# Performance work log

Measured on AMD Instinct MI355X. Metric: run time of the kernel, lower is better.

Reference implementation:

```python
import jax, jax.numpy as jnp
import numpy as np

D_MODEL = 1024
D_HEAD = 512
EPS = 1e-6


def setup_inputs() -> dict:
    key = jax.random.key(0)
    ks = jax.random.split(key, 12)
    s = 0.02
    B, T = 8, 2048
    return {
        "x": jax.random.normal(ks[0], (B, T, D_MODEL), dtype=jnp.float32),
        "norm_w": jnp.ones((D_MODEL,), dtype=jnp.float32),
        "Wq": jax.random.normal(ks[1], (D_HEAD, D_MODEL), dtype=jnp.float32) * s,
        "Wk": jax.random.normal(ks[2], (D_HEAD, D_MODEL), dtype=jnp.float32) * s,
        "Wv": jax.random.normal(ks[3], (D_HEAD, D_MODEL), dtype=jnp.float32) * s,
        "wi_w": jax.random.normal(ks[4], (1, D_MODEL), dtype=jnp.float32) * s,
        "wi_b": jnp.zeros((1,), dtype=jnp.float32),
        "wf_w": jax.random.normal(ks[5], (1, D_MODEL), dtype=jnp.float32) * s,
        "wf_b": jnp.zeros((1,), dtype=jnp.float32),
        "Wo": jax.random.normal(ks[6], (D_HEAD, D_MODEL), dtype=jnp.float32) * s,
        "bo": jnp.zeros((D_HEAD,), dtype=jnp.float32),
        "Wout": jax.random.normal(ks[7], (D_MODEL, D_HEAD), dtype=jnp.float32) * s,
    }


def _forward(x, norm_w, Wq, Wk, Wv, wi_w, wi_b, wf_w, wf_b, Wo, bo, Wout):
    B, T, d_model = x.shape
    d = Wq.shape[0]
    scale = 1.0 / jnp.sqrt(jnp.asarray(d, x.dtype))

    # RMSNorm (pre-norm)
    normed = x * jax.lax.rsqrt(jnp.mean(x * x, axis=-1, keepdims=True) + EPS) * norm_w

    # Precompute all per-timestep projections (vectorized over T)
    q = jnp.einsum('btm,dm->btd', normed, Wq) * scale  # (B,T,d)
    k = jnp.einsum('btm,dm->btd', normed, Wk) * scale
    v = jnp.einsum('btm,dm->btd', normed, Wv)
    zi = jnp.einsum('btm,m->bt', normed, wi_w[0]) + wi_b[0]  # (B,T)
    zf = jnp.einsum('btm,m->bt', normed, wf_w[0]) + wf_b[0]
    o = jax.nn.sigmoid(jnp.einsum('btm,dm->btd', normed, Wo) + bo)  # (B,T,d)

    # Time-major for scan
    qT = jnp.moveaxis(q, 1, 0)
    kT = jnp.moveaxis(k, 1, 0)
    vT = jnp.moveaxis(v, 1, 0)
    ziT = jnp.moveaxis(zi, 1, 0)
    zfT = jnp.moveaxis(zf, 1, 0)
    oT = jnp.moveaxis(o, 1, 0)

    C0 = jnp.zeros((B, d, d), x.dtype)
    n0 = jnp.zeros((B, d), x.dtype)
    m0 = jnp.full((B,), -jnp.inf, x.dtype)

    def step(carry, inp):
        C, n, m = carry
        q_t, k_t, v_t, zi_t, zf_t, o_t = inp
        m_t = jnp.maximum(zf_t + m, zi_t)                      # (B,)
        i_p = jnp.exp(zi_t - m_t)
        f_p = jnp.exp(zf_t + m - m_t)
        C_t = f_p[:, None, None] * C + i_p[:, None, None] * (v_t[:, :, None] * k_t[:, None, :])
        n_t = f_p[:, None] * n + i_p[:, None] * k_t
        Cq = jnp.einsum('bij,bj->bi', C_t, q_t)                # (B,d)
        denom = jnp.maximum(jnp.abs(jnp.sum(n_t * q_t, axis=-1, keepdims=True)), 1.0)
        h = o_t * Cq / denom
        return (C_t, n_t, m_t), h

    (C_f, n_f, m_f), hT = jax.lax.scan(step, (C0, n0, m0), (qT, kT, vT, ziT, zfT, oT))
    h = jnp.moveaxis(hT, 0, 1)                                 # (B,T,d)
    out = x + jnp.einsum('btd,md->btm', h, Wout)
    return out


def reference(x, norm_w, Wq, Wk, Wv, wi_w, wi_b, wf_w, wf_b, Wo, bo, Wout):
    return _forward(x, norm_w, Wq, Wk, Wv, wi_w, wi_b, wf_w, wf_b, Wo, bo, Wout)
```

## Files before the change

### kernel.cpp

```cpp
#include <hip/hip_runtime.h>
#include <cstdint>
#include <cmath>

#define T_SEQ 2048
#define NBATCH 8
#define DM 1024
#define DH 512
#define MROWS (NBATCH * T_SEQ)
#define NC 16
#define CL 128

typedef short s8v __attribute__((ext_vector_type(8)));
typedef float f32x4 __attribute__((ext_vector_type(4)));

typedef unsigned int __attribute__((address_space(1))) uint_g;
typedef unsigned int __attribute__((address_space(3))) uint_l;

#define QKSCALE 0.044194173824159216f

__device__ __forceinline__ float b2f(unsigned short s) {
    union { unsigned u; float f; } c; c.u = ((unsigned)s) << 16; return c.f;
}
__device__ __forceinline__ unsigned short f2b(float f) {
    union { float f; unsigned u; } c; c.f = f;
    unsigned r = c.u + 0x7fffu + ((c.u >> 16) & 1u);
    return (unsigned short)(r >> 16);
}
__device__ __forceinline__ void gld_lds16(const void* g, void* l) {
    __builtin_amdgcn_global_load_lds((const uint_g*)g, (uint_l*)l, 16, 0, 0);
}

#define WAITV(N) asm volatile("s_waitcnt vmcnt(" #N ")" ::: "memory")
#define BARSYNC() do { asm volatile("" ::: "memory"); __builtin_amdgcn_s_barrier(); asm volatile("" ::: "memory"); } while (0)

__global__ __launch_bounds__(256) void norm_kernel(
    const float* __restrict__ x, const float* __restrict__ nw,
    const float* __restrict__ wi, const float* __restrict__ wf,
    const float* __restrict__ wib, const float* __restrict__ wfb,
    unsigned short* __restrict__ normed, float* __restrict__ zi, float* __restrict__ zf,
    const float* __restrict__ Wq, const float* __restrict__ Wk,
    const float* __restrict__ Wo, const float* __restrict__ Wv,
    const float* __restrict__ Wout,
    unsigned short* __restrict__ Wcat1, unsigned short* __restrict__ WvB,
    unsigned short* __restrict__ Woutb)
{
    int t = blockIdx.x, tid = threadIdx.x;
    float4 xv = ((const float4*)(x + (size_t)t * DM))[tid];
    float ss = xv.x * xv.x + xv.y * xv.y + xv.z * xv.z + xv.w * xv.w;
#pragma unroll
    for (int m = 1; m < 64; m <<= 1) ss += __shfl_xor(ss, m, 64);
    __shared__ float sred[4];
    __shared__ float sred2[8];
    if ((tid & 63) == 0) sred[tid >> 6] = ss;
    __syncthreads();
    ss = sred[0] + sred[1] + sred[2] + sred[3];
    float rstd = rsqrtf(ss * (1.0f / DM) + 1e-6f);
    float4 nwv = ((const float4*)nw)[tid];
    float n0 = xv.x * rstd * nwv.x, n1 = xv.y * rstd * nwv.y;
    float n2 = xv.z * rstd * nwv.z, n3 = xv.w * rstd * nwv.w;
    ushort4 pk;
    pk.x = f2b(n0); pk.y = f2b(n1); pk.z = f2b(n2); pk.w = f2b(n3);
    ((ushort4*)(normed + (size_t)t * DM))[tid] = pk;
    float4 wiv = ((const float4*)wi)[tid];
    float4 wfv = ((const float4*)wf)[tid];
    float pzi = n0 * wiv.x + n1 * wiv.y + n2 * wiv.z + n3 * wiv.w;
    float pzf = n0 * wfv.x + n1 * wfv.y + n2 * wfv.z + n3 * wfv.w;
#pragma unroll
    for (int m = 1; m < 64; m <<= 1) {
        pzi += __shfl_xor(pzi, m, 64);
        pzf += __shfl_xor(pzf, m, 64);
    }
    if ((tid & 63) == 0) { sred2[tid >> 6] = pzi; sred2[4 + (tid >> 6)] = pzf; }
    __syncthreads();
    if (tid == 0) {
        zi[t] = sred2[0] + sred2[1] + sred2[2] + sred2[3] + wib[0];
        zf[t] = sred2[4] + sred2[5] + sred2[6] + sred2[7] + wfb[0];
    }
    if (tid < 160) {
        int idx = blockIdx.x * 160 + tid;
        if (idx < 1572864) {
            int nrow = idx >> 10;
            float v;
            if      (nrow < 512)  v = Wq[idx];
            else if (nrow < 1024) v = Wk[idx - 512 * 1024];
            else                  v = Wo[idx - 1024 * 1024];
            Wcat1[idx] = f2b(v);
        } else if (idx < 2097152) {
            int j = idx - 1572864;
            WvB[j] = f2b(Wv[j]);
        } else {
            int j = idx - 2097152;
            Woutb[j] = f2b(Wout[j]);
        }
    }
}

__global__ __launch_bounds__(256, 4) void gemm_qkv_ms(
    const unsigned short* __restrict__ normed, const unsigned short* __restrict__ Wcat1,
    const unsigned short* __restrict__ WvB, int K,
    unsigned short* __restrict__ qko, const float* __restrict__ bo,
    unsigned short* __restrict__ vout,
    const float* __restrict__ zi, const float* __restrict__ zf,
    float* __restrict__ u, float* __restrict__ a)
{
    __shared__ unsigned short As[128 * 64];
    __shared__ unsigned short Bs[128 * 64];
    __shared__ float wt[4];
    int tid = threadIdx.x;

    if (blockIdx.x >= 2048) {
        int b = blockIdx.x - 2048, lane = tid & 63, wid = tid >> 6;
        size_t base = (size_t)b * T_SEQ + tid * 8;
        float z_f[8], z_i[8];
        *(float4*)&z_f[0] = *(const float4*)&zf[base];
        *(float4*)&z_f[4] = *(const float4*)&zf[base + 4];
        *(float4*)&z_i[0] = *(const float4*)&zi[base];
        *(float4*)&z_i[4] = *(const float4*)&zi[base + 4];
        float c8[8]; float run = 0.0f;
#pragma unroll
        for (int i = 0; i < 8; ++i) { run += z_f[i]; c8[i] = run; }
        float v = run;
#pragma unroll
        for (int d = 1; d < 64; d <<= 1) {
            float o = __shfl_up(v, d, 64);
            if (lane >= d) v += o;
        }
        if (lane == 63) wt[wid] = v;
        __syncthreads();
        float woff = 0.0f;
        for (int j = 0; j < wid; ++j) woff += wt[j];
        float excl = __shfl_up(v, 1, 64);
        if (lane == 0) excl = 0.0f;
        float pre = woff + excl;
        float uu[8];
#pragma unroll
        for (int i = 0; i < 8; ++i) uu[i] = z_i[i] - (pre + c8[i]);
        *(float4*)&u[base] = *(float4*)&uu[0];
        *(float4*)&u[base + 4] = *(float4*)&uu[4];
        __syncthreads();
        float m8[8]; float rm = -INFINITY;
#pragma unroll
        for (int i = 0; i < 8; ++i) { rm = fmaxf(rm, uu[i]); m8[i] = rm; }
        float mv = rm;
#pragma unroll
        for (int d = 1; d < 64; d <<= 1) {
            float o = __shfl_up(mv, d, 64);
            if (lane >= d) mv = fmaxf(mv, o);
        }
        if (lane == 63) wt[wid] = mv;
        __syncthreads();
        float moff = -INFINITY;
        for (int j = 0; j < wid; ++j) moff = fmaxf(moff, wt[j]);
        float mexcl = __shfl_up(mv, 1, 64);
        if (lane == 0) mexcl = -INFINITY;
        float mpre = fmaxf(moff, mexcl);
        float aa[8];
#pragma unroll
        for (int i = 0; i < 8; ++i) aa[i] = fmaxf(mpre, m8[i]);
        *(float4*)&a[base] = *(float4*)&aa[0];
        *(float4*)&a[base + 4] = *(float4*)&aa[4];
        return;
    }

    int l = tid & 63, w = tid >> 6;
    int wg = (blockIdx.x & 7) * 256 + (blockIdx.x >> 3);
    int job = (wg >= 1536) ? 1 : 0;
    const unsigned short* A;
    const unsigned short* Bw;
    int bm, bn;
    if (job == 0) { A = normed; Bw = Wcat1; bn = wg % 12; bm = wg / 12; }
    else          { int w2 = wg - 1536; A = WvB; Bw = normed; bm = w2 & 3; bn = w2 >> 2; }
    int wr = w >> 1, wc = w & 1;
    f32x4 acc[4][4] = {};
    const size_t abase = (size_t)(bm * 128) * K;
    const size_t bbase = (size_t)(bn * 128) * K;

    for (int ks = 0; ks < K; ks += 64) {
        __syncthreads();
#pragma unroll
        for (int i = 0; i < 4; ++i) {
            int off = (i * 256 + tid) * 8;
            int row = off >> 6, kc = off & 63;
            int kcs = kc ^ ((row & 7) << 3);
            gld_lds16(A + abase + (size_t)row * K + ks + kcs, &As[off]);
            gld_lds16(Bw + bbase + (size_t)row * K + ks + kcs, &Bs[off]);
        }
        __syncthreads();
#pragma unroll
        for (int kk = 0; kk < 2; ++kk) {
            int cbo = kk * 32 + (l >> 4) * 8;
            s8v af[4], bfv[4];
#pragma unroll
            for (int m = 0; m < 4; ++m) {
                int row = wr * 64 + m * 16 + (l & 15);
                af[m] = *(const s8v*)&As[row * 64 + (cbo ^ ((row & 7) << 3))];
            }
#pragma unroll
            for (int n = 0; n < 4; ++n) {
                int row = wc * 64 + n * 16 + (l & 15);
                bfv[n] = *(const s8v*)&Bs[row * 64 + (cbo ^ ((row & 7) << 3))];
            }
#pragma unroll
            for (int m = 0; m < 4; ++m)
#pragma unroll
                for (int n = 0; n < 4; ++n)
                    acc[m][n] = __builtin_amdgcn_mfma_f32_16x16x32_bf16(af[m], bfv[n], acc[m][n], 0, 0, 0);
        }
    }

    if (job == 0) {
#pragma unroll
        for (int m = 0; m < 4; ++m) {
#pragma unroll
            for (int n = 0; n < 4; ++n) {
                int col = bn * 128 + wc * 64 + n * 16 + (l & 15);
#pragma unroll
                for (int r = 0; r < 4; ++r) {
                    int row = bm * 128 + wr * 64 + m * 16 + (l >> 4) * 4 + r;
                    float v = acc[m][n][r];
                    if (col < 1024) v *= QKSCALE;
                    else {
                        float s = v + bo[col - 1024];
                        v = 1.0f / (1.0f + expf(-s));
                    }
                    qko[(size_t)row * 1536 + col] = f2b(v);
                }
            }
        }
    } else {
#pragma unroll
        for (int m = 0; m < 4; ++m) {
#pragma unroll
            for (int n = 0; n < 4; ++n) {
                int col = bn * 128 + wc * 64 + n * 16 + (l & 15);
#pragma unroll
                for (int r = 0; r < 4; ++r) {
                    int row = bm * 128 + wr * 64 + m * 16 + (l >> 4) * 4 + r;
                    vout[(size_t)row * MROWS + col] = f2b(acc[m][n][r]);
                }
            }
        }
    }
}

template <int EPI, int ORD>
__global__ __launch_bounds__(256, 4) void gemm_bt(
    const unsigned short* __restrict__ A, const unsigned short* __restrict__ Bw,
    int M, int N, int K, int ldo,
    unsigned short* __restrict__ outb, const float* __restrict__ bo,
    float* __restrict__ outf, const float* __restrict__ xres)
{
    __shared__ unsigned short As[128 * 64];
    __shared__ unsigned short Bs[128 * 64];
    int tid = threadIdx.x;
    int l = tid & 63, w = tid >> 6;
    int cpx = gridDim.x >> 3;
    int wg = (blockIdx.x & 7) * cpx + (blockIdx.x >> 3);
    int mb = M >> 7;
    int nb = N >> 7;
    int bm, bn;
    if (ORD == 0) { bm = wg % mb; bn = wg / mb; }
    else          { bn = wg % nb; bm = wg / nb; }
    int wr = w >> 1, wc = w & 1;
    f32x4 acc[4][4] = {};
    const size_t abase = (size_t)(bm * 128) * K;
    const size_t bbase = (size_t)(bn * 128) * K;

    for (int ks = 0; ks < K; ks += 64) {
        __syncthreads();
#pragma unroll
        for (int i = 0; i < 4; ++i) {
            int off = (i * 256 + tid) * 8;
            int row = off >> 6, kc = off & 63;
            int kcs = kc ^ ((row & 7) << 3);
            gld_lds16(A + abase + (size_t)row * K + ks + kcs, &As[off]);
            gld_lds16(Bw + bbase + (size_t)row * K + ks + kcs, &Bs[off]);
        }
        __syncthreads();
#pragma unroll
        for (int kk = 0; kk < 2; ++kk) {
            int cbo = kk * 32 + (l >> 4) * 8;
            s8v af[4], bfv[4];
#pragma unroll
            for (int m = 0; m < 4; ++m) {
                int row = wr * 64 + m * 16 + (l & 15);
                af[m] = *(const s8v*)&As[row * 64 + (cbo ^ ((row & 7) << 3))];
            }
#pragma unroll
            for (int n = 0; n < 4; ++n) {
                int row = wc * 64 + n * 16 + (l & 15);
                bfv[n] = *(const s8v*)&Bs[row * 64 + (cbo ^ ((row & 7) << 3))];
            }
#pragma unroll
            for (int m = 0; m < 4; ++m)
#pragma unroll
                for (int n = 0; n < 4; ++n)
                    acc[m][n] = __builtin_amdgcn_mfma_f32_16x16x32_bf16(af[m], bfv[n], acc[m][n], 0, 0, 0);
        }
    }

#pragma unroll
    for (int m = 0; m < 4; ++m) {
#pragma unroll
        for (int n = 0; n < 4; ++n) {
            int col = bn * 128 + wc * 64 + n * 16 + (l & 15);
#pragma unroll
            for (int r = 0; r < 4; ++r) {
                int row = bm * 128 + wr * 64 + m * 16 + (l >> 4) * 4 + r;
                float v = acc[m][n][r];
                if (EPI == 3) {
                    outb[(size_t)row * ldo + col] = f2b(v);
                } else {
                    size_t idx = (size_t)row * ldo + col;
                    outf[idx] = xres[idx] + v;
                }
            }
        }
    }
}

__global__ __launch_bounds__(256) void fusedA_kernel(
    const unsigned short* __restrict__ qko,
    const float* __restrict__ u, const float* __restrict__ a,
    unsigned short* __restrict__ stb, float* __restrict__ rowsum,
    unsigned short* __restrict__ kw, float* __restrict__ P, float* __restrict__ aE)
{
    __shared__ char smem[17920];
    int bid = blockIdx.x, tid = threadIdx.x;

    if (bid < 256) {
        unsigned short* Qs = (unsigned short*)smem;
        unsigned short* Ks = (unsigned short*)(smem + 4096);
        int b = bid & 7, c = (bid >> 3) & 15, th = bid >> 7;
        int l = tid & 63, wv = tid >> 6;
        size_t cb = (size_t)b * T_SEQ + c * CL;
        f32x4 acc[8] = {};
        for (int ks = 0; ks < 512; ks += 32) {
            __syncthreads();
            {
                int p = tid;
                int row = p >> 2, kc = (p & 3) * 8;
                gld_lds16(qko + (cb + th * 64 + row) * 1536 + ks + kc, &Qs[p * 8]);
#pragma unroll
                for (int rI = 0; rI < 2; ++rI) {
                    int pp = rI * 256 + tid;
                    int rw = pp >> 2, kk = (pp & 3) * 8;
                    gld_lds16(qko + (cb + rw) * 1536 + 512 + ks + kk, &Ks[pp * 8]);
                }
            }
            __syncthreads();
            s8v af = *(const s8v*)&Qs[(wv * 16 + (l & 15)) * 32 + (l >> 4) * 8];
#pragma unroll
            for (int n = 0; n < 8; ++n) {
                s8v bf = *(const s8v*)&Ks[(n * 16 + (l & 15)) * 32 + (l >> 4) * 8];
                acc[n] = __builtin_amdgcn_mfma_f32_16x16x32_bf16(af, bf, acc[n], 0, 0, 0);
            }
        }
        float rs[4] = {0.f, 0.f, 0.f, 0.f};
        size_t stbase = (size_t)(b * NC + c) * (CL * CL);
#pragma unroll
        for (int e = 0; e < 4; ++e) {
            int tl = th * 64 + wv * 16 + (l >> 4) * 4 + e;
            float a_t = a[cb + tl];
#pragma unroll
            for (int n = 0; n < 8; ++n) {
                int j = n * 16 + (l & 15);
                float val = (j <= tl) ? acc[n][e] * expf(u[cb + j] - a_t) : 0.0f;
                rs[e] += val;
                stb[stbase + (size_t)tl * CL + j] = f2b(val);
            }
        }
#pragma unroll
        for (int e = 0; e < 4; ++e) {
#pragma unroll
            for (int m = 1; m < 16; m <<= 1) rs[e] += __shfl_xor(rs[e], m, 64);
        }
        if ((l & 15) == 0) {
#pragma unroll
            for (int e = 0; e < 4; ++e)
                rowsum[cb + th * 64 + wv * 16 + (l >> 4) * 4 + e] = rs[e];
        }
    } else {
        unsigned short (*T)[136] = (unsigned short(*)[136])smem;
        float* w_l = (float*)(smem + 17408);
        int kb = bid - 256;
        int b = kb & 7, c = (kb >> 3) & 15, stt = kb >> 7;
        int s0 = stt * 64;
        size_t cb = (size_t)b * T_SEQ + c * CL;
        float a_e = a[cb + CL - 1];
        if (tid < CL) w_l[tid] = expf(u[cb + tid] - a_e);
        if (tid == 0 && stt == 0) aE[b * NC + c] = a_e;
#pragma unroll
        for (int it = 0; it < 4; ++it) {
            int flat = it * 256 + tid;
            int t = flat >> 3, g = flat & 7;
            s8v v = *(const s8v*)&qko[(cb + t) * 1536 + 512 + s0 + g * 8];
#pragma unroll
            for (int e = 0; e < 8; ++e) T[g * 8 + e][t] = (unsigned short)v[e];
        }
        __syncthreads();
        int s = tid >> 2, tg = tid & 3;
        float psum = 0.0f;
#pragma unroll
        for (int j = 0; j < 4; ++j) {
            int t0 = tg * 32 + j * 8;
            s8v kv = *(const s8v*)&T[s][t0];
            s8v kwv;
#pragma unroll
            for (int e = 0; e < 8; ++e) {
                float f = b2f((unsigned short)kv[e]) * w_l[t0 + e];
                kwv[e] = (short)f2b(f);
                psum += f;
            }
            *(s8v*)&kw[(size_t)(s0 + s) * MROWS + cb + t0] = kwv;
        }
        psum += __shfl_xor(psum, 1, 64);
        psum += __shfl_xor(psum, 2, 64);
        if (tg == 0) P[(size_t)(b * NC + c) * 512 + s0 + s] = psum;
    }
}

__global__ __launch_bounds__(256, 2) void cscan3_kernel(
    const unsigned short* __restrict__ kvT, const unsigned short* __restrict__ kw,
    const float* __restrict__ aE, unsigned short* __restrict__ chk,
    const unsigned short* __restrict__ qko, const float* __restrict__ P,
    const float* __restrict__ a, const float* __restrict__ rowsum,
    float* __restrict__ rdnm)
{
    __shared__ unsigned short Vs[2][64 * 128];
    __shared__ unsigned short Ks[2][64 * 128];
    int bid = blockIdx.x;
    int b = bid & 7, rt = (bid >> 3) & 7, st = bid >> 6;
    int r0 = rt * 64, s0 = st * 64;
    int tid = threadIdx.x, l = tid & 63;
    int w = tid >> 6, wr = w >> 1, wc = w & 1;
    size_t tb = (size_t)b * T_SEQ;
    int srow = tid >> 4, sg = tid & 15;
    f32x4 acc[2][2] = {};
    float a_prev = 0.0f;

#define CSTAGE(c, buf) do { \
        size_t cb_ = tb + (size_t)(c) * CL; \
        _Pragma("unroll") \
        for (int i = 0; i < 4; ++i) { \
            int row_ = i * 16 + srow; \
            int gs_ = sg ^ (row_ & 7); \
            gld_lds16(kvT + (size_t)(512 + r0 + row_) * MROWS + cb_ + gs_ * 8, \
                      &Vs[buf][(i * 256 + tid) * 8]); \
        } \
        _Pragma("unroll") \
        for (int i = 0; i < 4; ++i) { \
            int row_ = i * 16 + srow; \
            int gs_ = sg ^ (row_ & 7); \
            gld_lds16(kw + (size_t)(s0 + row_) * MROWS + cb_ + gs_ * 8, \
                      &Ks[buf][(i * 256 + tid) * 8]); \
        } } while (0)

    CSTAGE(0, 0);
    for (int c = 0; c < NC; ++c) {
        int cur = c & 1;
        if (c + 1 < NC) { CSTAGE(c + 1, cur ^ 1); WAITV(8); }
        else            { WAITV(0); }
        BARSYNC();
        float a_e = aE[b * NC + c];
        if (c > 0) {
            unsigned short* slot = chk + (size_t)(b * (NC - 1) + (c - 1)) * (512 * 512);
#pragma unroll
            for (int m = 0; m < 2; ++m)
#pragma unroll
                for (int n = 0; n < 2; ++n)
#pragma unroll
                    for (int e = 0; e < 4; ++e) {
                        int r = r0 + wr * 32 + m * 16 + (l >> 4) * 4 + e;
                        int s = s0 + wc * 32 + n * 16 + (l & 15);
                        slot[r * 512 + s] = f2b(acc[m][n][e]);
                    }
            float gam = expf(a_prev - a_e);
#pragma unroll
            for (int m = 0; m < 2; ++m)
#pragma unroll
                for (int n = 0; n < 2; ++n)
#pragma unroll
                    for (int e = 0; e < 4; ++e) acc[m][n][e] *= gam;
        }
#pragma unroll
        for (int ks = 0; ks < 4; ++ks) {
            s8v vf[2], kf[2];
#pragma unroll
            for (int m = 0; m < 2; ++m) {
                int row = wr * 32 + m * 16 + (l & 15);
                int gf = ks * 4 + (l >> 4);
                vf[m] = *(const s8v*)&Vs[cur][row * 128 + ((gf ^ (row & 7)) << 3)];
            }
#pragma unroll
            for (int n = 0; n < 2; ++n) {
                int row = wc * 32 + n * 16 + (l & 15);
                int gf = ks * 4 + (l >> 4);
                kf[n] = *(const s8v*)&Ks[cur][row * 128 + ((gf ^ (row & 7)) << 3)];
            }
#pragma unroll
            for (int m = 0; m < 2; ++m)
#pragma unroll
                for (int n = 0; n < 2; ++n)
                    acc[m][n] = __builtin_amdgcn_mfma_f32_16x16x32_bf16(vf[m], kf[n], acc[m][n], 0, 0, 0);
        }
        a_prev = a_e;
        BARSYNC();
    }
#undef CSTAGE

    {
        int wv = tid >> 6;
        int t0 = bid * 32 + wv * 8;
        int bt = t0 >> 11, ct = (t0 & 2047) >> 7;
        float nh[8] = {0, 0, 0, 0, 0, 0, 0, 0};
        float aprev = 0.0f;
        for (int cp = 0; cp < ct; ++cp) {
            float ae = aE[bt * NC + cp];
            float gam = (cp == 0) ? 0.0f : expf(aprev - ae);
            const float* Pp = P + (size_t)(bt * NC + cp) * 512 + l * 8;
            float4 p0 = *(const float4*)Pp;
            float4 p1 = *(const float4*)(Pp + 4);
#pragma unroll
            for (int e = 0; e < 8; ++e) nh[e] *= gam;
            nh[0] += p0.x; nh[1] += p0.y; nh[2] += p0.z; nh[3] += p0.w;
            nh[4] += p1.x; nh[5] += p1.y; nh[6] += p1.z; nh[7] += p1.w;
            aprev = ae;
        }
        float aeprev = (ct > 0) ? aE[bt * NC + ct - 1] : 0.0f;
        for (int tt = 0; tt < 8; ++tt) {
            int tc = t0 + tt;
            s8v qv = *(const s8v*)(qko + (size_t)tc * 1536 + l * 8);
            float nq = 0.0f;
#pragma unroll
            for (int e = 0; e < 8; ++e) nq += b2f((unsigned short)qv[e]) * nh[e];
#pragma unroll
            for (int m = 1; m < 64; m <<= 1) nq += __shfl_xor(nq, m, 64);
            if (l == 0) {
                float beta = (ct == 0) ? 0.0f : expf(aeprev - a[tc]);
                rdnm[tc] = 1.0f / fmaxf(fabsf(beta * nq + rowsum[tc]), 1.0f);
            }
        }
    }
}

__global__ __launch_bounds__(512) void hout2_kernel(
    const unsigned short* __restrict__ qko, const unsigned short* __restrict__ kvT,
    const unsigned short* __restrict__ st, const unsigned short* __restrict__ chk,
    const float* __restrict__ a, const float* __restrict__ aE,
    const float* __restrict__ rdnm, unsigned short* __restrict__ g)
{
    __shared__ unsigned short Bsh[2][256 * 64];
    int bid = blockIdx.x;
    int b = bid & 7, cc = bid >> 3;
    int c = cc >> 1, rh = cc & 1;
    int tid = threadIdx.x, l = tid & 63, wv = tid >> 6;
    int mq = wv & 3, rg = wv >> 2;
    int rr = rg * 128 + rh * 256;
    int R0 = rh * 256;
    size_t cb = (size_t)b * T_SEQ + c * CL;
    f32x4 acc[2][8] = {};

    int srow7 = tid >> 3;
    int sgc = tid & 7;

    if (c > 0) {
        const unsigned short* slot = chk + (size_t)(b * (NC - 1) + (c - 1)) * (512 * 512);
#define HSTG_C(ksb, buf) do { \
        _Pragma("unroll") \
        for (int i = 0; i < 4; ++i) { \
            int row_ = i * 64 + srow7; \
            int gs_ = sgc ^ (row_ & 7); \
            gld_lds16(slot + (size_t)(R0 + row_) * 512 + (ksb) * 64 + gs_ * 8, \
                      &Bsh[buf][(i * 512 + tid) * 8]); \
        } } while (0)
        HSTG_C(0, 0);
        for (int s = 0; s < 8; ++s) {
            int cur = s & 1;
            if (s + 1 < 8) { HSTG_C(s + 1, cur ^ 1); WAITV(4); }
            else           { WAITV(0); }
            BARSYNC();
#pragma unroll
            for (int kk = 0; kk < 2; ++kk) {
                s8v aq[2];
#pragma unroll
                for (int mf = 0; mf < 2; ++mf)
                    aq[mf] = *(const s8v*)&qko[(cb + mq * 32 + mf * 16 + (l & 15)) * 1536 + s * 64 + kk * 32 + (l >> 4) * 8];
#pragma unroll
                for (int n = 0; n < 8; ++n) {
                    int row = rg * 128 + n * 16 + (l & 15);
                    int gr = (kk * 4 + (l >> 4)) ^ (row & 7);
                    s8v bc = *(const s8v*)&Bsh[cur][row * 64 + gr * 8];
                    acc[0][n] = __builtin_amdgcn_mfma_f32_16x16x32_bf16(aq[0], bc, acc[0][n], 0, 0, 0);
                    acc[1][n] = __builtin_amdgcn_mfma_f32_16x16x32_bf16(aq[1], bc, acc[1][n], 0, 0, 0);
                }
            }
            BARSYNC();
        }
#undef HSTG_C
        float aprev = aE[b * NC + c - 1];
#pragma unroll
        for (int mf = 0; mf < 2; ++mf)
#pragma unroll
            for (int e = 0; e < 4; ++e) {
                int t = mq * 32 + mf * 16 + (l >> 4) * 4 + e;
                float bta = expf(aprev - a[cb + t]);
#pragma unroll
                for (int n = 0; n < 8; ++n) acc[mf][n][e] *= bta;
            }
    }

    const unsigned short* stp = st + (size_t)(b * NC + c) * (CL * CL);
#define HSTG_V(vsb, buf) do { \
        _Pragma("unroll") \
        for (int i = 0; i < 4; ++i) { \
            int row_ = i * 64 + srow7; \
            int gs_ = sgc ^ (row_ & 7); \
            gld_lds16(kvT + (size_t)(512 + R0 + row_) * MROWS + cb + (vsb) * 64 + gs_ * 8, \
                      &Bsh[buf][(i * 512 + tid) * 8]); \
        } } while (0)
    HSTG_V(0, 0);
    for (int s = 0; s < 2; ++s) {
        if (s + 1 < 2) { HSTG_V(1, 1); WAITV(4); }
        else           { WAITV(0); }
        BARSYNC();
#pragma unroll
        for (int kk = 0; kk < 2; ++kk) {
            s8v aq[2];
#pragma unroll
            for (int mf = 0; mf < 2; ++mf)
                aq[mf] = *(const s8v*)&stp[(size_t)(mq * 32 + mf * 16 + (l & 15)) * CL + s * 64 + kk * 32 + (l >> 4) * 8];
#pragma unroll
            for (int n = 0; n < 8; ++n) {
                int row = rg * 128 + n * 16 + (l & 15);
                int gr = (kk * 4 + (l >> 4)) ^ (row & 7);
                s8v bv = *(const s8v*)&Bsh[s][row * 64 + gr * 8];
                acc[0][n] = __builtin_amdgcn_mfma_f32_16x16x32_bf16(aq[0], bv, acc[0][n], 0, 0, 0);
                acc[1][n] = __builtin_amdgcn_mfma_f32_16x16x32_bf16(aq[1], bv, acc[1][n], 0, 0, 0);
            }
        }
        BARSYNC();
    }
#undef HSTG_V

#pragma unroll
    for (int mf = 0; mf < 2; ++mf)
#pragma unroll
        for (int e = 0; e < 4; ++e) {
            int t = mq * 32 + mf * 16 + (l >> 4) * 4 + e;
            float rd = rdnm[cb + t];
#pragma unroll
            for (int n = 0; n < 8; ++n) {
                int r = rr + n * 16 + (l & 15);
                float ov = b2f(qko[(cb + t) * 1536 + 1024 + r]);
                g[(cb + t) * DH + r] = f2b(ov * acc[mf][n][e] * rd);
            }
        }
}

extern "C" void kernel_launch(void* const* d_in, const int* in_sizes, int n_in,
                              void* d_out, int out_size, void* d_ws, size_t ws_size,
                              hipStream_t stream)
{
    (void)in_sizes; (void)n_in; (void)out_size; (void)ws_size;
    const float* x    = (const float*)d_in[0];
    const float* nw   = (const float*)d_in[1];
    const float* Wq   = (const float*)d_in[2];
    const float* Wk   = (const float*)d_in[3];
    const float* Wv   = (const float*)d_in[4];
    const float* wi   = (const float*)d_in[5];
    const float* wib  = (const float*)d_in[6];
    const float* wf   = (const float*)d_in[7];
    const float* wfb  = (const float*)d_in[8];
    const float* Wo   = (const float*)d_in[9];
    const float* bo   = (const float*)d_in[10];
    const float* Wout = (const float*)d_in[11];
    float* out = (float*)d_out;

    char* ws = (char*)d_ws;
    unsigned short* qko    = (unsigned short*)ws;
    unsigned short* kvT    = (unsigned short*)(ws + 50331648);
    unsigned short* normed = (unsigned short*)(ws + 83886080);
    unsigned short* g      = normed;
    unsigned short* kw     = (unsigned short*)(ws + 100663296);
    float* Pbuf   = (float*)(ws + 117440512);
    float* aE     = (float*)(ws + 117964800);
    unsigned short* Wcat1  = (unsigned short*)(ws + 117440512);
    unsigned short* WvB    = (unsigned short*)(ws + 120586240);
    unsigned short* Woutb  = (unsigned short*)(ws + 122683392);
    float* zi     = (float*)(ws + 123731968);
    float* zf     = zi + MROWS;
    float* uarr   = zf + MROWS;
    float* aarr   = uarr + MROWS;
    float* rowsum = aarr + MROWS;
    float* rdnm   = rowsum + MROWS;

    unsigned short* chk   = (unsigned short*)d_out;
    unsigned short* stbuf = (unsigned short*)((char*)d_out + 62914560);

    norm_kernel    <<<MROWS, 256, 0, stream>>>(x, nw, wi, wf, wib, wfb, normed, zi, zf,
                                               Wq, Wk, Wo, Wv, Wout, Wcat1, WvB, Woutb);
    gemm_qkv_ms    <<<2056, 256, 0, stream>>>(normed, Wcat1, WvB, DM, qko, bo,
                                              kvT + (size_t)512 * MROWS, zi, zf, uarr, aarr);
    fusedA_kernel  <<<1280, 256, 0, stream>>>(qko, uarr, aarr, stbuf, rowsum, kw, Pbuf, aE);
    cscan3_kernel  <<<512, 256, 0, stream>>>(kvT, kw, aE, chk, qko, Pbuf, aarr, rowsum, rdnm);
    hout2_kernel   <<<256, 512, 0, stream>>>(qko, kvT, stbuf, chk, aarr, aE, rdnm, g);
    gemm_bt<1, 1>  <<<128 * 8, 256, 0, stream>>>(g, Woutb, MROWS, DM, DH, DM, nullptr, nullptr, out, x);
}
```

Before: 243.6 us.

## Regroup chunk kernels: move intra-chunk QK into scan kernel, denominators into output kernel

```diff
diff --git a/kernel.cpp b/kernel.cpp
--- a/kernel.cpp
+++ b/kernel.cpp
@@ -319,43 +319,105 @@
     }
 }
 
-__global__ __launch_bounds__(256) void fusedA_kernel(
+__global__ __launch_bounds__(256) void kwprep2_kernel(
     const unsigned short* __restrict__ qko,
     const float* __restrict__ u, const float* __restrict__ a,
-    unsigned short* __restrict__ stb, float* __restrict__ rowsum,
     unsigned short* __restrict__ kw, float* __restrict__ P, float* __restrict__ aE)
 {
-    __shared__ char smem[17920];
-    int bid = blockIdx.x, tid = threadIdx.x;
-
-    if (bid < 256) {
+    __shared__ unsigned short T[64][136];
+    __shared__ float w_l[CL];
+    int bid = blockIdx.x;
+    int b = bid & 7, c = (bid >> 3) & 15, stt = bid >> 7;
+    int s0 = stt * 64;
+    int tid = threadIdx.x;
+    size_t cb = (size_t)b * T_SEQ + c * CL;
+    float a_e = a[cb + CL - 1];
+    if (tid < CL) w_l[tid] = expf(u[cb + tid] - a_e);
+    if (tid == 0 && stt == 0) aE[b * NC + c] = a_e;
+#pragma unroll
+    for (int it = 0; it < 4; ++it) {
+        int flat = it * 256 + tid;
+        int t = flat >> 3, g = flat & 7;
+        s8v v = *(const s8v*)&qko[(cb + t) * 1536 + 512 + s0 + g * 8];
+#pragma unroll
+        for (int e = 0; e < 8; ++e) T[g * 8 + e][t] = (unsigned short)v[e];
+    }
+    __syncthreads();
+    int s = tid >> 2, tg = tid & 3;
+    float psum = 0.0f;
+#pragma unroll
+    for (int j = 0; j < 4; ++j) {
+        int t0 = tg * 32 + j * 8;
+        s8v kv = *(const s8v*)&T[s][t0];
+        s8v kwv;
+#pragma unroll
+        for (int e = 0; e < 8; ++e) {
+            float f = b2f((unsigned short)kv[e]) * w_l[t0 + e];
+            kwv[e] = (short)f2b(f);
+            psum += f;
+        }
+        *(s8v*)&kw[(size_t)(s0 + s) * MROWS + cb + t0] = kwv;
+    }
+    psum += __shfl_xor(psum, 1, 64);
+    psum += __shfl_xor(psum, 2, 64);
+    if (tg == 0) P[(size_t)(b * NC + c) * 512 + s0 + s] = psum;
+}
+
+__global__ __launch_bounds__(256, 2) void fusedB_kernel(
+    const unsigned short* __restrict__ kvT, const unsigned short* __restrict__ kw,
+    const float* __restrict__ aE, unsigned short* __restrict__ chk,
+    const unsigned short* __restrict__ qko,
+    const float* __restrict__ u, const float* __restrict__ a,
+    unsigned short* __restrict__ stb, float* __restrict__ rowsum)
+{
+    __shared__ char smem[65536];
+    int bid = blockIdx.x, tid = threadIdx.x, l = tid & 63;
+
+    if (bid % 3 == 2) {
+        int pid = bid / 3;
         unsigned short* Qs = (unsigned short*)smem;
-        unsigned short* Ks = (unsigned short*)(smem + 4096);
-        int b = bid & 7, c = (bid >> 3) & 15, th = bid >> 7;
-        int l = tid & 63, wv = tid >> 6;
+        unsigned short* Ks = (unsigned short*)(smem + 16384);
+        int b = pid & 7, c = (pid >> 3) & 15, th = pid >> 7;
+        int wv = tid >> 6;
         size_t cb = (size_t)b * T_SEQ + c * CL;
         f32x4 acc[8] = {};
-        for (int ks = 0; ks < 512; ks += 32) {
-            __syncthreads();
-            {
-                int p = tid;
-                int row = p >> 2, kc = (p & 3) * 8;
-                gld_lds16(qko + (cb + th * 64 + row) * 1536 + ks + kc, &Qs[p * 8]);
-#pragma unroll
-                for (int rI = 0; rI < 2; ++rI) {
-                    int pp = rI * 256 + tid;
-                    int rw = pp >> 2, kk = (pp & 3) * 8;
-                    gld_lds16(qko + (cb + rw) * 1536 + 512 + ks + kk, &Ks[pp * 8]);
+#define PSTAGE(s, buf) do { \
+        int ksb = (s) * 64; \
+        _Pragma("unroll") \
+        for (int i = 0; i < 2; ++i) { \
+            int gq = i * 256 + tid; int row = gq >> 3, gc = gq & 7; \
+            int kcs = (gc << 3) ^ ((row & 7) << 3); \
+            gld_lds16(qko + (cb + th * 64 + row) * 1536 + ksb + kcs, \
+                      &Qs[(buf) * 4096 + gq * 8]); } \
+        _Pragma("unroll") \
+        for (int i = 0; i < 4; ++i) { \
+            int gk = i * 256 + tid; int row = gk >> 3, gc = gk & 7; \
+            int kcs = (gc << 3) ^ ((row & 7) << 3); \
+            gld_lds16(qko + (cb + row) * 1536 + 512 + ksb + kcs, \
+                      &Ks[(buf) * 8192 + gk * 8]); } \
+        } while (0)
+        PSTAGE(0, 0);
+        for (int s = 0; s < 8; ++s) {
+            int cur = s & 1;
+            if (s + 1 < 8) { PSTAGE(s + 1, cur ^ 1); WAITV(6); }
+            else           { WAITV(0); }
+            BARSYNC();
+#pragma unroll
+            for (int kc = 0; kc < 2; ++kc) {
+                int row_a = wv * 16 + (l & 15);
+                int ga = (kc * 4 + (l >> 4)) ^ (row_a & 7);
+                s8v af = *(const s8v*)&Qs[cur * 4096 + row_a * 64 + ga * 8];
+#pragma unroll
+                for (int n = 0; n < 8; ++n) {
+                    int row_b = n * 16 + (l & 15);
+                    int gb = (kc * 4 + (l >> 4)) ^ (row_b & 7);
+                    s8v bf = *(const s8v*)&Ks[cur * 8192 + row_b * 64 + gb * 8];
+                    acc[n] = __builtin_amdgcn_mfma_f32_16x16x32_bf16(af, bf, acc[n], 0, 0, 0);
                 }
             }
-            __syncthreads();
-            s8v af = *(const s8v*)&Qs[(wv * 16 + (l & 15)) * 32 + (l >> 4) * 8];
-#pragma unroll
-            for (int n = 0; n < 8; ++n) {
-                s8v bf = *(const s8v*)&Ks[(n * 16 + (l & 15)) * 32 + (l >> 4) * 8];
-                acc[n] = __builtin_amdgcn_mfma_f32_16x16x32_bf16(af, bf, acc[n], 0, 0, 0);
-            }
-        }
+            BARSYNC();
+        }
+#undef PSTAGE
         float rs[4] = {0.f, 0.f, 0.f, 0.f};
         size_t stbase = (size_t)(b * NC + c) * (CL * CL);
 #pragma unroll
@@ -380,59 +442,14 @@
             for (int e = 0; e < 4; ++e)
                 rowsum[cb + th * 64 + wv * 16 + (l >> 4) * 4 + e] = rs[e];
         }
-    } else {
-        unsigned short (*T)[136] = (unsigned short(*)[136])smem;
-        float* w_l = (float*)(smem + 17408);
-        int kb = bid - 256;
-        int b = kb & 7, c = (kb >> 3) & 15, stt = kb >> 7;
-        int s0 = stt * 64;
-        size_t cb = (size_t)b * T_SEQ + c * CL;
-        float a_e = a[cb + CL - 1];
-        if (tid < CL) w_l[tid] = expf(u[cb + tid] - a_e);
-        if (tid == 0 && stt == 0) aE[b * NC + c] = a_e;
-#pragma unroll
-        for (int it = 0; it < 4; ++it) {
-            int flat = it * 256 + tid;
-            int t = flat >> 3, g = flat & 7;
-            s8v v = *(const s8v*)&qko[(cb + t) * 1536 + 512 + s0 + g * 8];
-#pragma unroll
-            for (int e = 0; e < 8; ++e) T[g * 8 + e][t] = (unsigned short)v[e];
-        }
-        __syncthreads();
-        int s = tid >> 2, tg = tid & 3;
-        float psum = 0.0f;
-#pragma unroll
-        for (int j = 0; j < 4; ++j) {
-            int t0 = tg * 32 + j * 8;
-            s8v kv = *(const s8v*)&T[s][t0];
-            s8v kwv;
-#pragma unroll
-            for (int e = 0; e < 8; ++e) {
-                float f = b2f((unsigned short)kv[e]) * w_l[t0 + e];
-                kwv[e] = (short)f2b(f);
-                psum += f;
-            }
-            *(s8v*)&kw[(size_t)(s0 + s) * MROWS + cb + t0] = kwv;
-        }
-        psum += __shfl_xor(psum, 1, 64);
-        psum += __shfl_xor(psum, 2, 64);
-        if (tg == 0) P[(size_t)(b * NC + c) * 512 + s0 + s] = psum;
-    }
-}
-
-__global__ __launch_bounds__(256, 2) void cscan3_kernel(
-    const unsigned short* __restrict__ kvT, const unsigned short* __restrict__ kw,
-    const float* __restrict__ aE, unsigned short* __restrict__ chk,
-    const unsigned short* __restrict__ qko, const float* __restrict__ P,
-    const float* __restrict__ a, const float* __restrict__ rowsum,
-    float* __restrict__ rdnm)
-{
-    __shared__ unsigned short Vs[2][64 * 128];
-    __shared__ unsigned short Ks[2][64 * 128];
-    int bid = blockIdx.x;
-    int b = bid & 7, rt = (bid >> 3) & 7, st = bid >> 6;
+        return;
+    }
+
+    int cid = (bid / 3) * 2 + (bid % 3);
+    unsigned short* Vs = (unsigned short*)smem;
+    unsigned short* Ks = (unsigned short*)(smem + 32768);
+    int b = cid & 7, rt = (cid >> 3) & 7, st = cid >> 6;
     int r0 = rt * 64, s0 = st * 64;
-    int tid = threadIdx.x, l = tid & 63;
     int w = tid >> 6, wr = w >> 1, wc = w & 1;
     size_t tb = (size_t)b * T_SEQ;
     int srow = tid >> 4, sg = tid & 15;
@@ -446,14 +463,14 @@
             int row_ = i * 16 + srow; \
             int gs_ = sg ^ (row_ & 7); \
             gld_lds16(kvT + (size_t)(512 + r0 + row_) * MROWS + cb_ + gs_ * 8, \
-                      &Vs[buf][(i * 256 + tid) * 8]); \
+                      &Vs[(buf) * 8192 + (i * 256 + tid) * 8]); \
         } \
         _Pragma("unroll") \
         for (int i = 0; i < 4; ++i) { \
             int row_ = i * 16 + srow; \
             int gs_ = sg ^ (row_ & 7); \
             gld_lds16(kw + (size_t)(s0 + row_) * MROWS + cb_ + gs_ * 8, \
-                      &Ks[buf][(i * 256 + tid) * 8]); \
+                      &Ks[(buf) * 8192 + (i * 256 + tid) * 8]); \
         } } while (0)
 
     CSTAGE(0, 0);
@@ -490,13 +507,13 @@
             for (int m = 0; m < 2; ++m) {
                 int row = wr * 32 + m * 16 + (l & 15);
                 int gf = ks * 4 + (l >> 4);
-                vf[m] = *(const s8v*)&Vs[cur][row * 128 + ((gf ^ (row & 7)) << 3)];
+                vf[m] = *(const s8v*)&Vs[cur * 8192 + row * 128 + ((gf ^ (row & 7)) << 3)];
             }
 #pragma unroll
             for (int n = 0; n < 2; ++n) {
                 int row = wc * 32 + n * 16 + (l & 15);
                 int gf = ks * 4 + (l >> 4);
-                kf[n] = *(const s8v*)&Ks[cur][row * 128 + ((gf ^ (row & 7)) << 3)];
+                kf[n] = *(const s8v*)&Ks[cur * 8192 + row * 128 + ((gf ^ (row & 7)) << 3)];
             }
 #pragma unroll
             for (int m = 0; m < 2; ++m)
@@ -508,49 +525,17 @@
         BARSYNC();
     }
 #undef CSTAGE
-
-    {
-        int wv = tid >> 6;
-        int t0 = bid * 32 + wv * 8;
-        int bt = t0 >> 11, ct = (t0 & 2047) >> 7;
-        float nh[8] = {0, 0, 0, 0, 0, 0, 0, 0};
-        float aprev = 0.0f;
-        for (int cp = 0; cp < ct; ++cp) {
-            float ae = aE[bt * NC + cp];
-            float gam = (cp == 0) ? 0.0f : expf(aprev - ae);
-            const float* Pp = P + (size_t)(bt * NC + cp) * 512 + l * 8;
-            float4 p0 = *(const float4*)Pp;
-            float4 p1 = *(const float4*)(Pp + 4);
-#pragma unroll
-            for (int e = 0; e < 8; ++e) nh[e] *= gam;
-            nh[0] += p0.x; nh[1] += p0.y; nh[2] += p0.z; nh[3] += p0.w;
-            nh[4] += p1.x; nh[5] += p1.y; nh[6] += p1.z; nh[7] += p1.w;
-            aprev = ae;
-        }
-        float aeprev = (ct > 0) ? aE[bt * NC + ct - 1] : 0.0f;
-        for (int tt = 0; tt < 8; ++tt) {
-            int tc = t0 + tt;
-            s8v qv = *(const s8v*)(qko + (size_t)tc * 1536 + l * 8);
-            float nq = 0.0f;
-#pragma unroll
-            for (int e = 0; e < 8; ++e) nq += b2f((unsigned short)qv[e]) * nh[e];
-#pragma unroll
-            for (int m = 1; m < 64; m <<= 1) nq += __shfl_xor(nq, m, 64);
-            if (l == 0) {
-                float beta = (ct == 0) ? 0.0f : expf(aeprev - a[tc]);
-                rdnm[tc] = 1.0f / fmaxf(fabsf(beta * nq + rowsum[tc]), 1.0f);
-            }
-        }
-    }
-}
-
-__global__ __launch_bounds__(512) void hout2_kernel(
+}
+
+__global__ __launch_bounds__(512) void hout3_kernel(
     const unsigned short* __restrict__ qko, const unsigned short* __restrict__ kvT,
     const unsigned short* __restrict__ st, const unsigned short* __restrict__ chk,
     const float* __restrict__ a, const float* __restrict__ aE,
-    const float* __restrict__ rdnm, unsigned short* __restrict__ g)
+    const float* __restrict__ P, const float* __restrict__ rowsum,
+    unsigned short* __restrict__ g)
 {
     __shared__ unsigned short Bsh[2][256 * 64];
+    __shared__ float rdl[CL];
     int bid = blockIdx.x;
     int b = bid & 7, cc = bid >> 3;
     int c = cc >> 1, rh = cc & 1;
@@ -560,6 +545,38 @@
     int R0 = rh * 256;
     size_t cb = (size_t)b * T_SEQ + c * CL;
     f32x4 acc[2][8] = {};
+
+    if (wv < 4) {
+        float nh[8] = {0, 0, 0, 0, 0, 0, 0, 0};
+        float aprev = 0.0f;
+        for (int cp = 0; cp < c; ++cp) {
+            float ae = aE[b * NC + cp];
+            float gam = (cp == 0) ? 0.0f : expf(aprev - ae);
+            const float* Pp = P + (size_t)(b * NC + cp) * 512 + l * 8;
+            float4 p0 = *(const float4*)Pp;
+            float4 p1 = *(const float4*)(Pp + 4);
+#pragma unroll
+            for (int e = 0; e < 8; ++e) nh[e] *= gam;
+            nh[0] += p0.x; nh[1] += p0.y; nh[2] += p0.z; nh[3] += p0.w;
+            nh[4] += p1.x; nh[5] += p1.y; nh[6] += p1.z; nh[7] += p1.w;
+            aprev = ae;
+        }
+        float aeprev = (c > 0) ? aE[b * NC + c - 1] : 0.0f;
+        for (int tt = 0; tt < 32; ++tt) {
+            int tloc = wv * 32 + tt;
+            s8v qv = *(const s8v*)(qko + (cb + tloc) * 1536 + l * 8);
+            float nq = 0.0f;
+#pragma unroll
+            for (int e = 0; e < 8; ++e) nq += b2f((unsigned short)qv[e]) * nh[e];
+#pragma unroll
+            for (int m = 1; m < 64; m <<= 1) nq += __shfl_xor(nq, m, 64);
+            if (l == 0) {
+                float beta = (c == 0) ? 0.0f : expf(aeprev - a[cb + tloc]);
+                rdl[tloc] = 1.0f / fmaxf(fabsf(beta * nq + rowsum[cb + tloc]), 1.0f);
+            }
+        }
+    }
+    BARSYNC();
 
     int srow7 = tid >> 3;
     int sgc = tid & 7;
@@ -648,7 +665,7 @@
 #pragma unroll
         for (int e = 0; e < 4; ++e) {
             int t = mq * 32 + mf * 16 + (l >> 4) * 4 + e;
-            float rd = rdnm[cb + t];
+            float rd = rdl[t];
 #pragma unroll
             for (int n = 0; n < 8; ++n) {
                 int r = rr + n * 16 + (l & 15);
@@ -693,7 +710,6 @@
     float* uarr   = zf + MROWS;
     float* aarr   = uarr + MROWS;
     float* rowsum = aarr + MROWS;
-    float* rdnm   = rowsum + MROWS;
 
     unsigned short* chk   = (unsigned short*)d_out;
     unsigned short* stbuf = (unsigned short*)((char*)d_out + 62914560);
@@ -702,8 +718,8 @@
                                                Wq, Wk, Wo, Wv, Wout, Wcat1, WvB, Woutb);
     gemm_qkv_ms    <<<2056, 256, 0, stream>>>(normed, Wcat1, WvB, DM, qko, bo,
                                               kvT + (size_t)512 * MROWS, zi, zf, uarr, aarr);
-    fusedA_kernel  <<<1280, 256, 0, stream>>>(qko, uarr, aarr, stbuf, rowsum, kw, Pbuf, aE);
-    cscan3_kernel  <<<512, 256, 0, stream>>>(kvT, kw, aE, chk, qko, Pbuf, aarr, rowsum, rdnm);
-    hout2_kernel   <<<256, 512, 0, stream>>>(qko, kvT, stbuf, chk, aarr, aE, rdnm, g);
+    kwprep2_kernel <<<1024, 256, 0, stream>>>(qko, uarr, aarr, kw, Pbuf, aE);
+    fusedB_kernel  <<<768, 256, 0, stream>>>(kvT, kw, aE, chk, qko, uarr, aarr, stbuf, rowsum);
+    hout3_kernel   <<<256, 512, 0, stream>>>(qko, kvT, stbuf, chk, aarr, aE, Pbuf, rowsum, g);
     gemm_bt<1, 1>  <<<128 * 8, 256, 0, stream>>>(g, Woutb, MROWS, DM, DH, DM, nullptr, nullptr, out, x);
 }
```

After: 262.1 us. 1.08x slower.
